# Kernel optimization log

Measured on AMD Instinct MI355X. Metric: run time of the kernel, lower is better.

## Reference

```python
import jax, jax.numpy as jnp
import numpy as np

VERY_NEG = -1e30
N_HEADS = 8


def _dag_attention(leaves, ancestors, mask, w1, b1, w2, b2):
    # leaves/ancestors: [C, A, H], mask: [C, A]
    m = mask[..., None]                                   # [C, A, 1]
    x = jnp.concatenate([leaves * m, ancestors * m], -1)  # [C, A, 2H]
    x = jax.nn.relu(x @ w1 + b1)                          # [C, A, H]
    s = x @ w2 + b2 + (1.0 - m) * VERY_NEG                # [C, A, 1]
    a = jax.nn.softmax(s, axis=1)
    return (a * ancestors * m).sum(axis=1)                # [C, H]


def _encoder_layer(x, mask4d, wq, wk, wv, wo, fw1, fb1, fw2, fb2):
    B, S, H = x.shape
    d = H // N_HEADS
    q = (x @ wq).reshape(B, S, N_HEADS, d)
    k = (x @ wk).reshape(B, S, N_HEADS, d)
    v = (x @ wv).reshape(B, S, N_HEADS, d)
    scores = jnp.einsum('bqhd,bkhd->bhqk', q, k) / jnp.sqrt(jnp.float32(d)) + mask4d
    attn = jax.nn.softmax(scores, axis=-1)
    ctx = jnp.einsum('bhqk,bkhd->bqhd', attn, v).reshape(B, S, H)
    x = x + ctx @ wo
    x = x + jax.nn.relu(x @ fw1 + fb1) @ fw2 + fb2
    return x


def _attention_pooling(x, mask3d, pw, pb):
    # x: [B, S, H], mask3d: [B, S, 1] additive mask
    s = x @ pw + pb + mask3d           # [B, S, 1]
    a = jax.nn.softmax(s, axis=1)
    return (a * x).sum(axis=1)          # [B, H]


def setup_inputs() -> dict:
    key = jax.random.key(0)
    ks = jax.random.split(key, 32)
    B, S, H, C, NODES, A = 128, 256, 256, 20000, 25000, 8

    def w(k, shape, scale=0.02):
        return (jax.random.normal(k, shape, jnp.float32) * scale)

    input_ids = jax.random.randint(ks[0], (B, S), 0, C)
    code_mask = (jax.random.uniform(ks[1], (B, S)) < 0.9).astype(jnp.float32)
    code_mask = code_mask.at[:, 0].set(1.0)
    dx_leaves_list = jax.random.randint(ks[2], (C, A), 0, NODES)
    dx_ancestors_list = jax.random.randint(ks[3], (C, A), 0, NODES)
    dx_masks_list = (jax.random.uniform(ks[4], (C, A)) < 0.8).astype(jnp.float32)
    dx_masks_list = dx_masks_list.at[:, 0].set(1.0)

    inp = dict(
        input_ids=input_ids, code_mask=code_mask,
        dx_leaves_list=dx_leaves_list, dx_ancestors_list=dx_ancestors_list,
        dx_masks_list=dx_masks_list,
        embed_init_w=w(ks[5], (NODES + 1, H)).at[NODES].set(0.0),  # padding row
        embed_inputs_w=w(ks[6], (C + 1, H)).at[C].set(0.0),
        attn_w1=w(ks[7], (2 * H, H)), attn_b1=jnp.zeros((H,), jnp.float32),
        attn_w2=w(ks[8], (H, 1)), attn_b2=jnp.zeros((1,), jnp.float32),
        pool_w=w(ks[9], (H, 1)), pool_b=jnp.zeros((1,), jnp.float32),
    )
    names = ['visit', 'dag']
    for i, nm in enumerate(names):
        base = 10 + 6 * i
        inp[nm + '_wq'] = w(ks[base], (H, H))
        inp[nm + '_wk'] = w(ks[base + 1], (H, H))
        inp[nm + '_wv'] = w(ks[base + 2], (H, H))
        inp[nm + '_wo'] = w(ks[base + 3], (H, H))
        inp[nm + '_fw1'] = w(ks[base + 4], (H, 4 * H))
        inp[nm + '_fb1'] = jnp.zeros((4 * H,), jnp.float32)
        inp[nm + '_fw2'] = w(ks[base + 5], (4 * H, H))
        inp[nm + '_fb2'] = jnp.zeros((H,), jnp.float32)
    return inp


def reference(input_ids, code_mask, dx_leaves_list, dx_ancestors_list, dx_masks_list,
              embed_init_w, embed_inputs_w, attn_w1, attn_b1, attn_w2, attn_b2,
              pool_w, pool_b,
              visit_wq, visit_wk, visit_wv, visit_wo, visit_fw1, visit_fb1, visit_fw2, visit_fb2,
              dag_wq, dag_wk, dag_wv, dag_wo, dag_fw1, dag_fb1, dag_fw2, dag_fb2):
    H = embed_init_w.shape[1]
    # Full-vocabulary DAG embedding recomputation (gather -> MLP -> masked softmax -> weighted sum)
    leaves_emb = embed_init_w[dx_leaves_list]          # [C, A, H]
    ancestors_emb = embed_init_w[dx_ancestors_list]    # [C, A, H]
    dag_emb = _dag_attention(leaves_emb, ancestors_emb, dx_masks_list,
                             attn_w1, attn_b1, attn_w2, attn_b2)   # [C, H]
    dict_matrix = jnp.concatenate([jnp.zeros((1, H), jnp.float32), dag_emb], axis=0)

    inputs = embed_inputs_w[input_ids]       # [B, S, H]
    inputs_dag = dict_matrix[input_ids]      # [B, S, H]

    ext_mask = (1.0 - code_mask)[:, None, None, :] * VERY_NEG  # [B,1,1,S]
    visit_outs = _encoder_layer(inputs, ext_mask, visit_wq, visit_wk, visit_wv, visit_wo,
                                visit_fw1, visit_fb1, visit_fw2, visit_fb2)
    dag_hidden = _encoder_layer(inputs_dag, ext_mask, dag_wq, dag_wk, dag_wv, dag_wo,
                                dag_fw1, dag_fb1, dag_fw2, dag_fb2)

    pool_mask = (1.0 - code_mask)[:, :, None] * VERY_NEG       # [B,S,1]
    dag_outs = _attention_pooling(dag_hidden, pool_mask, pool_w, pool_b)
    return (visit_outs, dag_outs)
```

## Files before the change

kernel.cpp:

```cpp
#include <hip/hip_runtime.h>
#include <hip/hip_bf16.h>
#include <math.h>

#define VERY_NEG (-1e30f)

constexpr int Bc = 128, Sc = 256, Hc = 256, Cc = 20000, Ac = 8, NHc = 8, DHc = 32, FFc = 1024;
constexpr int Mc = Bc * Sc;
constexpr int Rc = Cc * Ac;

typedef __attribute__((ext_vector_type(8))) short short8;
typedef __attribute__((ext_vector_type(4))) float floatx4;

static __device__ __forceinline__ unsigned short f2bf(float f) {
  union { float f; unsigned u; } v; v.f = f;
  unsigned r = v.u + 0x7FFF + ((v.u >> 16) & 1);
  return (unsigned short)(r >> 16);
}
static __device__ __forceinline__ unsigned pack2(float lo, float hi) {
  return (unsigned)f2bf(lo) | ((unsigned)f2bf(hi) << 16);
}
static __device__ __forceinline__ float bf2f(unsigned short u) {
  union { unsigned u; float f; } v; v.u = ((unsigned)u) << 16; return v.f;
}

static __device__ __forceinline__ void glds16(const unsigned short* g,
                                              unsigned short* l) {
  __builtin_amdgcn_global_load_lds(
      (const __attribute__((address_space(1))) void*)g,
      (__attribute__((address_space(3))) void*)l, 16, 0, 0);
}

__global__ __launch_bounds__(256) void prep_weights(
    const float* __restrict__ wq, const float* __restrict__ wk,
    const float* __restrict__ wv, const float* __restrict__ wo,
    const float* __restrict__ fw1, const float* __restrict__ fw2,
    unsigned short* __restrict__ qkvT, unsigned short* __restrict__ woT,
    unsigned short* __restrict__ fw1T, unsigned short* __restrict__ fw2T) {
  int gid = blockIdx.x * 256 + threadIdx.x;
  if (gid < 196608) {
    int which = gid >> 16, rem = gid & 65535;
    int n = rem >> 8, k = rem & 255;
    const float* w = which == 0 ? wq : (which == 1 ? wk : wv);
    qkvT[gid] = f2bf(w[k * 256 + n]);
  } else if (gid < 262144) {
    int rem = gid - 196608;
    int n = rem >> 8, k = rem & 255;
    woT[rem] = f2bf(wo[k * 256 + n]);
  } else if (gid < 524288) {
    int rem = gid - 262144;
    int n = rem >> 8, k = rem & 255;
    fw1T[rem] = f2bf(fw1[k * 1024 + n]);
  } else {
    int rem = gid - 524288;
    int n = rem >> 10, k = rem & 1023;
    fw2T[rem] = f2bf(fw2[k * 256 + n]);
  }
}

template <int K, bool BIAS, bool RELU, bool RESID, int OUT>
__global__ __launch_bounds__(256) void gemm_mfma(
    const unsigned short* __restrict__ A, const unsigned short* __restrict__ Bt,
    const float* __restrict__ bias, const float* __restrict__ resid,
    float* __restrict__ Cf, unsigned short* __restrict__ C2, int N) {
  __shared__ unsigned short As[128 * 64];
  __shared__ unsigned short Bs[128 * 64];
  const int tid = threadIdx.x;
  const int nwg = gridDim.x * gridDim.y;
  const int bid0 = blockIdx.y * gridDim.x + blockIdx.x;
  const int swz = (bid0 & 7) * (nwg >> 3) + (bid0 >> 3);
  const int rowBase = (swz / gridDim.x) * 128;
  const int colBase = (swz % gridDim.x) * 128;
  const int wave = tid >> 6, lane = tid & 63;
  const int wm = wave >> 1, wn = wave & 1;
  const int quad = lane >> 4, l15 = lane & 15;
  const int s8 = (((lane & 7) ^ (lane >> 3)) << 3);
  const int rs0 = (wave << 5) + (lane >> 3);
  const int swzf = l15 & 7;

  floatx4 acc[4][4];
#pragma unroll
  for (int mt = 0; mt < 4; ++mt)
#pragma unroll
    for (int nt = 0; nt < 4; ++nt) acc[mt][nt] = (floatx4){0.f, 0.f, 0.f, 0.f};

  for (int k0 = 0; k0 < K; k0 += 64) {
#pragma unroll
    for (int i = 0; i < 4; ++i) {
      int r = rs0 + (i << 3);
      int lb = wave * 2048 + i * 512;
      glds16(A + (size_t)(rowBase + r) * K + k0 + s8, &As[lb]);
      glds16(Bt + (size_t)(colBase + r) * K + k0 + s8, &Bs[lb]);
    }
    __syncthreads();
#pragma unroll
    for (int kk = 0; kk < 2; ++kk) {
      short8 af[4], bfr[4];
#pragma unroll
      for (int mt = 0; mt < 4; ++mt)
        af[mt] = *(const short8*)&As[(wm * 64 + mt * 16 + l15) * 64 +
                                     ((((kk << 2) | quad) ^ swzf) << 3)];
#pragma unroll
      for (int nt = 0; nt < 4; ++nt)
        bfr[nt] = *(const short8*)&Bs[(wn * 64 + nt * 16 + l15) * 64 +
                                      ((((kk << 2) | quad) ^ swzf) << 3)];
#pragma unroll
      for (int mt = 0; mt < 4; ++mt)
#pragma unroll
        for (int nt = 0; nt < 4; ++nt)
          acc[mt][nt] = __builtin_amdgcn_mfma_f32_16x16x32_bf16(
              af[mt], bfr[nt], acc[mt][nt], 0, 0, 0);
    }
    __syncthreads();
  }

#pragma unroll
  for (int mt = 0; mt < 4; ++mt) {
#pragma unroll
    for (int nt = 0; nt < 4; ++nt) {
      int col = colBase + wn * 64 + nt * 16 + l15;
      float bz = BIAS ? bias[col] : 0.f;
#pragma unroll
      for (int i = 0; i < 4; ++i) {
        int row = rowBase + wm * 64 + mt * 16 + quad * 4 + i;
        float v = acc[mt][nt][i];
        if (BIAS) v += bz;
        if (RELU) v = fmaxf(v, 0.f);
        if (RESID) v += resid[(size_t)row * N + col];
        if (OUT == 0) {
          Cf[(size_t)row * N + col] = v;
        } else if (OUT == 1) {
          C2[(size_t)row * N + col] = f2bf(v);
        } else if (OUT == 2) {
          Cf[(size_t)row * N + col] = v;
          C2[(size_t)row * N + col] = f2bf(v);
        } else {
          C2[(size_t)(col >> 8) * 16777216 + (size_t)row * 256 + (col & 255)] =
              f2bf(v);
        }
      }
    }
  }
}

__global__ __launch_bounds__(256) void cvt_emb16(
    const float* __restrict__ emb, unsigned short* __restrict__ e16) {
  int gid = blockIdx.x * 256 + threadIdx.x;
  int base = gid * 8;
  int row = base >> 8;
  uint4 o;
  if (row < 25001) {
    float4 a = *(const float4*)(emb + base);
    float4 b = *(const float4*)(emb + base + 4);
    o.x = pack2(a.x, a.y); o.y = pack2(a.z, a.w);
    o.z = pack2(b.x, b.y); o.w = pack2(b.z, b.w);
  } else {
    o = (uint4){0u, 0u, 0u, 0u};
  }
  *(uint4*)(e16 + base) = o;
}

__global__ __launch_bounds__(256) void prep_w1T_pq(
    const float* __restrict__ w1, unsigned short* __restrict__ Bt) {
  int gid = blockIdx.x * 256 + threadIdx.x;
  int n = gid >> 8, k = gid & 255;
  float v = (n < 256) ? w1[k * 256 + n] : w1[(256 + k) * 256 + (n - 256)];
  Bt[gid] = f2bf(v);
}

__global__ __launch_bounds__(256) void dag_score(
    const int* __restrict__ leaves, const int* __restrict__ anc,
    const unsigned short* __restrict__ PQ, const float* __restrict__ b1,
    const float* __restrict__ w2, float* __restrict__ s) {
  const int tid = threadIdx.x;
  const int l16 = tid & 15;
  const int r = blockIdx.x * 16 + (tid >> 4);

  float b1c[16], w2c[16];
#pragma unroll
  for (int j = 0; j < 4; ++j) {
    *(float4*)&b1c[j * 4] = *(const float4*)(b1 + l16 * 16 + j * 4);
    *(float4*)&w2c[j * 4] = *(const float4*)(w2 + l16 * 16 + j * 4);
  }

  const int nl = leaves[r], na = anc[r];
  const unsigned short* pp = PQ + (size_t)nl * 512 + l16 * 16;
  const unsigned short* qp = PQ + (size_t)na * 512 + 256 + l16 * 16;

  float acc = 0.f;
#pragma unroll
  for (int half = 0; half < 2; ++half) {
    uint4 pv = *(const uint4*)(pp + half * 8);
    uint4 qv = *(const uint4*)(qp + half * 8);
    const unsigned short* pu = (const unsigned short*)&pv;
    const unsigned short* qu = (const unsigned short*)&qv;
#pragma unroll
    for (int j = 0; j < 8; ++j) {
      float h = bf2f(pu[j]) + bf2f(qu[j]) + b1c[half * 8 + j];
      acc += fmaxf(h, 0.f) * w2c[half * 8 + j];
    }
  }
  acc += __shfl_xor(acc, 1, 64);
  acc += __shfl_xor(acc, 2, 64);
  acc += __shfl_xor(acc, 4, 64);
  acc += __shfl_xor(acc, 8, 64);
  if (l16 == 0) s[r] = acc;
}

__global__ __launch_bounds__(256) void dag_finalize(
    const float* __restrict__ s, const float* __restrict__ masks,
    const int* __restrict__ anc, const float* __restrict__ b2,
    const unsigned short* __restrict__ emb16, float* __restrict__ dict) {
  const int c = blockIdx.x;
  const int t = threadIdx.x;
  __shared__ float sv[8], mv[8];
  __shared__ int nv[8];
  if (t < 8) {
    int idx = c * 8 + t;
    float m = masks[idx];
    sv[t] = s[idx] + b2[0] + (1.f - m) * VERY_NEG;
    mv[t] = m;
    nv[t] = anc[idx];
  }
  __syncthreads();
  float mx = -INFINITY;
#pragma unroll
  for (int a = 0; a < 8; ++a) mx = fmaxf(mx, sv[a]);
  float e[8], sum = 0.f;
#pragma unroll
  for (int a = 0; a < 8; ++a) { e[a] = __expf(sv[a] - mx); sum += e[a]; }
  float inv = 1.f / sum;
  float o = 0.f;
#pragma unroll
  for (int a = 0; a < 8; ++a)
    o += e[a] * inv * mv[a] * bf2f(emb16[(size_t)nv[a] * 256 + t]);
  dict[(size_t)(c + 1) * 256 + t] = o;
  if (c == 0) dict[t] = 0.f;
}

__global__ __launch_bounds__(256) void gather_both(
    const int* __restrict__ ids, const float4* __restrict__ table,
    float4* __restrict__ outf, unsigned short* __restrict__ outb) {
  int gid = blockIdx.x * 256 + threadIdx.x;
  int row = gid >> 6;
  int c4 = gid & 63;
  float4 v = table[(size_t)ids[row] * 64 + c4];
  outf[gid] = v;
  uint2 o;
  o.x = pack2(v.x, v.y);
  o.y = pack2(v.z, v.w);
  *(uint2*)(outb + (size_t)gid * 4) = o;
}

static __device__ __forceinline__ int vt_addr(int d, int col) {
  return d * 272 + ((((col) * 2) ^ (((d >> 3) & 3) << 4)) >> 1);
}
static __device__ __forceinline__ int ps_addr(int row, int col) {
  return row * 40 + ((((col) * 2) ^ (((row >> 2) & 3) << 4)) >> 1);
}

__global__ __launch_bounds__(256, 4) void attn_mfma(
    const unsigned short* __restrict__ q, const unsigned short* __restrict__ k,
    const unsigned short* __restrict__ v, const float* __restrict__ cm,
    unsigned short* __restrict__ ctx) {
  __shared__ unsigned short Vt[32 * 272];
  __shared__ unsigned short Ps[4][64 * 40];
  __shared__ float madd[256];
  const int b = blockIdx.x >> 3, h = blockIdx.x & 7;
  const int tid = threadIdx.x;
  const int wave = tid >> 6, lane = tid & 63;
  const int quad = lane >> 4, l15 = lane & 15;
  const size_t tokbase = (size_t)b * 256;
  const int hoff = h * 32;

#pragma unroll
  for (int it = 0; it < 4; ++it) {
    int idx = tid + it * 256;
    int row = idx >> 2, c = idx & 3;
    uint4 w = *(const uint4*)(v + (tokbase + row) * 256 + hoff + c * 8);
    const unsigned short* wsp = (const unsigned short*)&w;
#pragma unroll
    for (int j = 0; j < 8; ++j) Vt[vt_addr(c * 8 + j, row)] = wsp[j];
  }
  madd[tid] = (1.f - cm[b * 256 + tid]) * VERY_NEG;
  __syncthreads();

  short8 qf[4];
#pragma unroll
  for (int mt = 0; mt < 4; ++mt) {
    size_t qrow = tokbase + wave * 64 + mt * 16 + l15;
    qf[mt] = *(const short8*)(q + qrow * 256 + hoff + quad * 8);
  }
  float madd_r[16];
#pragma unroll
  for (int nt = 0; nt < 16; ++nt) madd_r[nt] = madd[nt * 16 + l15];

  short8 vone;
#pragma unroll
  for (int j = 0; j < 8; ++j)
    ((unsigned short*)&vone)[j] = (l15 == 0) ? 0x3F80 : 0;

  floatx4 oa[4][2], oa_l[4];
#pragma unroll
  for (int mt = 0; mt < 4; ++mt) {
    oa_l[mt] = (floatx4){0.f, 0.f, 0.f, 0.f};
#pragma unroll
    for (int nd = 0; nd < 2; ++nd) oa[mt][nd] = (floatx4){0.f, 0.f, 0.f, 0.f};
  }

  const float scale = 0.17677669529663687f;
  unsigned short* Pw = &Ps[wave][0];

  for (int t = 0; t < 4; ++t) {
    short8 kf[4];
#pragma unroll
    for (int nt = 0; nt < 4; ++nt)
      kf[nt] = *(const short8*)(k + (tokbase + t * 64 + nt * 16 + l15) * 256 +
                                hoff + quad * 8);
    floatx4 sa[4][4];
#pragma unroll
    for (int mt = 0; mt < 4; ++mt)
#pragma unroll
      for (int nt = 0; nt < 4; ++nt) sa[mt][nt] = (floatx4){0.f, 0.f, 0.f, 0.f};
#pragma unroll
    for (int mt = 0; mt < 4; ++mt)
#pragma unroll
      for (int nt = 0; nt < 4; ++nt)
        sa[mt][nt] = __builtin_amdgcn_mfma_f32_16x16x32_bf16(
            qf[mt], kf[nt], sa[mt][nt], 0, 0, 0);

#pragma unroll
    for (int ks = 0; ks < 2; ++ks) {
#pragma unroll
      for (int mt = 0; mt < 4; ++mt)
#pragma unroll
        for (int n2 = 0; n2 < 2; ++n2) {
          int nt = ks * 2 + n2;
#pragma unroll
          for (int i = 0; i < 4; ++i) {
            float p = __expf(sa[mt][nt][i] * scale + madd_r[t * 4 + nt]);
            Pw[ps_addr(mt * 16 + quad * 4 + i, n2 * 16 + l15)] = f2bf(p);
          }
        }
      __asm__ __volatile__("s_waitcnt lgkmcnt(0)" ::: "memory");
      short8 vf[2];
#pragma unroll
      for (int nd = 0; nd < 2; ++nd)
        vf[nd] = *(const short8*)&Vt[vt_addr(nd * 16 + l15,
                                             t * 64 + ks * 32 + quad * 8)];
#pragma unroll
      for (int mt = 0; mt < 4; ++mt) {
        short8 pf = *(const short8*)&Pw[ps_addr(mt * 16 + l15, quad * 8)];
#pragma unroll
        for (int nd = 0; nd < 2; ++nd)
          oa[mt][nd] = __builtin_amdgcn_mfma_f32_16x16x32_bf16(
              pf, vf[nd], oa[mt][nd], 0, 0, 0);
        oa_l[mt] = __builtin_amdgcn_mfma_f32_16x16x32_bf16(
            pf, vone, oa_l[mt], 0, 0, 0);
      }
    }
  }

  float inv[4][4];
#pragma unroll
  for (int mt = 0; mt < 4; ++mt)
#pragma unroll
    for (int i = 0; i < 4; ++i) {
      float l = __shfl(oa_l[mt][i], lane & 48, 64);
      inv[mt][i] = 1.f / l;
    }
#pragma unroll
  for (int mt = 0; mt < 4; ++mt)
#pragma unroll
    for (int nd = 0; nd < 2; ++nd)
#pragma unroll
      for (int i = 0; i < 4; ++i)
        Pw[ps_addr(mt * 16 + quad * 4 + i, nd * 16 + l15)] =
            f2bf(oa[mt][nd][i] * inv[mt][i]);
  __asm__ __volatile__("s_waitcnt lgkmcnt(0)" ::: "memory");
#pragma unroll
  for (int it = 0; it < 4; ++it) {
    int idx = it * 64 + lane;
    int row = idx >> 2, c = idx & 3;
    uint4 w = *(const uint4*)&Pw[ps_addr(row, c * 8)];
    *(uint4*)(ctx + (tokbase + wave * 64 + row) * 256 + hoff + c * 8) = w;
  }
}

__global__ __launch_bounds__(256) void pool_kernel(
    const float* __restrict__ x, const float* __restrict__ code_mask,
    const float* __restrict__ pw, const float* __restrict__ pb,
    float* __restrict__ out) {
  const int b = blockIdx.x;
  const int t = threadIdx.x;
  __shared__ float ss[256];
  __shared__ float red[256];
  __shared__ float als[256];
  const float* xb = x + (size_t)b * 256 * 256;

  float s = pb[0];
  for (int j = 0; j < 256; j += 4) {
    float4 xv = *(const float4*)(xb + (size_t)t * 256 + j);
    float4 wv = *(const float4*)(pw + j);
    s += xv.x * wv.x + xv.y * wv.y + xv.z * wv.z + xv.w * wv.w;
  }
  s += (1.f - code_mask[b * 256 + t]) * VERY_NEG;
  ss[t] = s; red[t] = s;
  __syncthreads();
  for (int off = 128; off > 0; off >>= 1) {
    if (t < off) red[t] = fmaxf(red[t], red[t + off]);
    __syncthreads();
  }
  float m = red[0];
  __syncthreads();
  float e = __expf(ss[t] - m);
  als[t] = e; red[t] = e;
  __syncthreads();
  for (int off = 128; off > 0; off >>= 1) {
    if (t < off) red[t] += red[t + off];
    __syncthreads();
  }
  float inv = 1.f / red[0];
  float o = 0.f;
  for (int si = 0; si < 256; ++si) o += als[si] * xb[(size_t)si * 256 + t];
  out[b * 256 + t] = o * inv;
}

extern "C" void kernel_launch(void* const* d_in, const int* in_sizes, int n_in,
                              void* d_out, int out_size, void* d_ws,
                              size_t ws_size, hipStream_t stream) {
  const int* input_ids = (const int*)d_in[0];
  const float* code_mask = (const float*)d_in[1];
  const int* dx_leaves = (const int*)d_in[2];
  const int* dx_anc = (const int*)d_in[3];
  const float* dx_masks = (const float*)d_in[4];
  const float* embed_init_w = (const float*)d_in[5];
  const float* embed_inputs_w = (const float*)d_in[6];
  const float* attn_w1 = (const float*)d_in[7];
  const float* attn_b1 = (const float*)d_in[8];
  const float* attn_w2 = (const float*)d_in[9];
  const float* attn_b2 = (const float*)d_in[10];
  const float* pool_w = (const float*)d_in[11];
  const float* pool_b = (const float*)d_in[12];

  float* out = (float*)d_out;
  float* ws = (float*)d_ws;

  float* dict = ws;
  float* xbuf = dict + 5120256;
  float* qb   = xbuf + 8388608;
  float* kb   = qb + 8388608;
  float* vb   = kb + 8388608;
  float* ctxb = vb + 8388608;
  float* wend = ctxb + 8388608;

  unsigned short* emb16  = (unsigned short*)xbuf;
  unsigned short* pq16   = (unsigned short*)(xbuf + 3211264);
  unsigned short* w1T_pq = (unsigned short*)kb;
  float* sbuf = vb;

  unsigned short* xb16  = (unsigned short*)ctxb;
  unsigned short* qkv16 = (unsigned short*)qb;
  unsigned short* xq16  = (unsigned short*)qb;
  unsigned short* hid16 = (unsigned short*)kb;
  unsigned short* qkvT = (unsigned short*)wend;
  unsigned short* woT  = qkvT + 196608;
  unsigned short* fw1T = woT + 65536;
  unsigned short* fw2T = fw1T + 262144;

  cvt_emb16<<<3136, 256, 0, stream>>>(embed_init_w, emb16);
  prep_w1T_pq<<<512, 256, 0, stream>>>(attn_w1, w1T_pq);
  gemm_mfma<256, false, false, false, 1><<<dim3(4, 196), 256, 0, stream>>>(
      emb16, w1T_pq, nullptr, nullptr, nullptr, pq16, 512);
  dag_score<<<Rc / 16, 256, 0, stream>>>(dx_leaves, dx_anc, pq16, attn_b1,
                                         attn_w2, sbuf);
  dag_finalize<<<Cc, 256, 0, stream>>>(sbuf, dx_masks, dx_anc, attn_b2,
                                       emb16, dict);

  auto run_encoder = [&](const float* wq, const float* wk, const float* wv,
                         const float* wo, const float* fw1, const float* fb1,
                         const float* fw2, const float* fb2, float* final_out) {
    prep_weights<<<3072, 256, 0, stream>>>(wq, wk, wv, wo, fw1, fw2, qkvT,
                                           woT, fw1T, fw2T);
    gemm_mfma<256, false, false, false, 3><<<dim3(6, 256), 256, 0, stream>>>(
        xb16, qkvT, nullptr, nullptr, nullptr, qkv16, 256);
    attn_mfma<<<Bc * NHc, 256, 0, stream>>>(qkv16, qkv16 + 16777216,
                                            qkv16 + 33554432, code_mask, xb16);
    gemm_mfma<256, false, false, true, 2><<<dim3(2, 256), 256, 0, stream>>>(
        xb16, woT, nullptr, xbuf, xbuf, xq16, 256);
    gemm_mfma<256, true, true, false, 1><<<dim3(8, 256), 256, 0, stream>>>(
        xq16, fw1T, fb1, nullptr, nullptr, hid16, 1024);
    gemm_mfma<1024, true, false, true, 0><<<dim3(2, 256), 256, 0, stream>>>(
        hid16, fw2T, fb2, xbuf, final_out, nullptr, 256);
  };

  gather_both<<<8192, 256, 0, stream>>>(input_ids,
                                        (const float4*)embed_inputs_w,
                                        (float4*)xbuf, xb16);
  run_encoder((const float*)d_in[13], (const float*)d_in[14],
              (const float*)d_in[15], (const float*)d_in[16],
              (const float*)d_in[17], (const float*)d_in[18],
              (const float*)d_in[19], (const float*)d_in[20], out);

  gather_both<<<8192, 256, 0, stream>>>(input_ids, (const float4*)dict,
                                        (float4*)xbuf, xb16);
  run_encoder((const float*)d_in[21], (const float*)d_in[22],
              (const float*)d_in[23], (const float*)d_in[24],
              (const float*)d_in[25], (const float*)d_in[26],
              (const float*)d_in[27], (const float*)d_in[28], xbuf);

  pool_kernel<<<Bc, 256, 0, stream>>>(xbuf, code_mask, pool_w, pool_b,
                                      out + 8388608);
}
```

Baseline: 536.5 us.

## Fuse FFN up and down GEMMs into one kernel keeping hidden in LDS

Replaces the two FFN GEMM launches with a single kernel that computes each 128-row block's 1024-wide hidden activation in 128-column chunks, stores the chunk in shared memory, and immediately accumulates the down-projection. This removes the global write and re-read of the 32768x1024 bf16 hidden tensor. The cost is only 256 blocks at one block per CU with heavy register use (128 accumulator floats plus the hidden tile) and many barriers, so latency hiding is limited. The pooling kernel is also widened to 512 threads, splitting the weighted sum over sequence positions into two halves.

```diff
diff --git a/kernel.cpp b/kernel.cpp
--- a/kernel.cpp
+++ b/kernel.cpp
@@ -142,6 +142,158 @@
   }
 }
 
+__global__ __launch_bounds__(256, 1) void ffn_fused(
+    const unsigned short* __restrict__ A, const unsigned short* __restrict__ w1T,
+    const unsigned short* __restrict__ w2T, const float* __restrict__ b1,
+    const float* __restrict__ b2, const float* __restrict__ resid,
+    float* __restrict__ outC) {
+  __shared__ unsigned short Xs[4][8192];
+  __shared__ unsigned short Ws[2][8192];
+  __shared__ unsigned short Hs[2][8192];
+  const int tid = threadIdx.x;
+  const int wave = tid >> 6, lane = tid & 63;
+  const int wm = wave >> 1, wn = wave & 1;
+  const int quad = lane >> 4, l15 = lane & 15;
+  const int s8 = (((lane & 7) ^ (lane >> 3)) << 3);
+  const int rs0 = (wave << 5) + (lane >> 3);
+  const int rs0b = (wave << 6) + (lane >> 3);
+  const int swzf = l15 & 15 & 7;
+  const int rowBase = blockIdx.x * 128;
+
+#pragma unroll
+  for (int kc = 0; kc < 4; ++kc)
+#pragma unroll
+    for (int i = 0; i < 4; ++i) {
+      int r = rs0 + (i << 3);
+      glds16(A + (size_t)(rowBase + r) * 256 + kc * 64 + s8,
+             &Xs[kc][wave * 2048 + i * 512]);
+    }
+
+  floatx4 acc2[4][8];
+#pragma unroll
+  for (int mt = 0; mt < 4; ++mt)
+#pragma unroll
+    for (int nt = 0; nt < 8; ++nt) acc2[mt][nt] = (floatx4){0.f, 0.f, 0.f, 0.f};
+
+  for (int nb = 0; nb < 8; ++nb) {
+    floatx4 hacc[4][4];
+#pragma unroll
+    for (int mt = 0; mt < 4; ++mt)
+#pragma unroll
+      for (int nt = 0; nt < 4; ++nt) hacc[mt][nt] = (floatx4){0.f, 0.f, 0.f, 0.f};
+
+#pragma unroll
+    for (int hf = 0; hf < 2; ++hf) {
+#pragma unroll
+      for (int kc = 0; kc < 2; ++kc)
+#pragma unroll
+        for (int i = 0; i < 4; ++i) {
+          int r = rs0 + (i << 3);
+          glds16(w1T + (size_t)(nb * 128 + r) * 256 + (hf * 2 + kc) * 64 + s8,
+                 &Ws[kc][wave * 2048 + i * 512]);
+        }
+      __syncthreads();
+#pragma unroll
+      for (int kc = 0; kc < 2; ++kc) {
+        int kg = hf * 2 + kc;
+#pragma unroll
+        for (int kk = 0; kk < 2; ++kk) {
+          short8 af[4], bfr[4];
+#pragma unroll
+          for (int mt = 0; mt < 4; ++mt)
+            af[mt] = *(const short8*)&Xs[kg][(wm * 64 + mt * 16 + l15) * 64 +
+                                            ((((kk << 2) | quad) ^ swzf) << 3)];
+#pragma unroll
+          for (int nt = 0; nt < 4; ++nt)
+            bfr[nt] = *(const short8*)&Ws[kc][(wn * 64 + nt * 16 + l15) * 64 +
+                                             ((((kk << 2) | quad) ^ swzf) << 3)];
+#pragma unroll
+          for (int mt = 0; mt < 4; ++mt)
+#pragma unroll
+            for (int nt = 0; nt < 4; ++nt)
+              hacc[mt][nt] = __builtin_amdgcn_mfma_f32_16x16x32_bf16(
+                  af[mt], bfr[nt], hacc[mt][nt], 0, 0, 0);
+        }
+      }
+      __syncthreads();
+    }
+
+    float b1v[4];
+#pragma unroll
+    for (int nt = 0; nt < 4; ++nt)
+      b1v[nt] = b1[nb * 128 + wn * 64 + nt * 16 + l15];
+#pragma unroll
+    for (int mt = 0; mt < 4; ++mt)
+#pragma unroll
+      for (int nt = 0; nt < 4; ++nt) {
+        int nh = wn * 64 + nt * 16 + l15;
+        int kc2 = nh >> 6, c6 = nh & 63;
+#pragma unroll
+        for (int i = 0; i < 4; ++i) {
+          int row = wm * 64 + mt * 16 + quad * 4 + i;
+          float hv = fmaxf(hacc[mt][nt][i] + b1v[nt], 0.f);
+          Hs[kc2][row * 64 + ((((c6 >> 3) ^ (row & 7)) << 3) | (c6 & 7))] =
+              f2bf(hv);
+        }
+      }
+#pragma unroll
+    for (int i = 0; i < 8; ++i) {
+      int r = rs0b + (i << 3);
+      glds16(w2T + (size_t)r * 1024 + nb * 128 + s8,
+             &Ws[0][wave * 4096 + i * 512]);
+    }
+    __syncthreads();
+
+#pragma unroll
+    for (int kc2 = 0; kc2 < 2; ++kc2) {
+      if (kc2 == 1) {
+        __syncthreads();
+#pragma unroll
+        for (int i = 0; i < 8; ++i) {
+          int r = rs0b + (i << 3);
+          glds16(w2T + (size_t)r * 1024 + nb * 128 + 64 + s8,
+                 &Ws[0][wave * 4096 + i * 512]);
+        }
+        __syncthreads();
+      }
+#pragma unroll
+      for (int kk = 0; kk < 2; ++kk) {
+        short8 pf[4], bfr2[8];
+#pragma unroll
+        for (int mt = 0; mt < 4; ++mt)
+          pf[mt] = *(const short8*)&Hs[kc2][(wm * 64 + mt * 16 + l15) * 64 +
+                                           ((((kk << 2) | quad) ^ swzf) << 3)];
+        const unsigned short* W2f = &Ws[0][0];
+#pragma unroll
+        for (int nt = 0; nt < 8; ++nt)
+          bfr2[nt] = *(const short8*)&W2f[(wn * 128 + nt * 16 + l15) * 64 +
+                                          ((((kk << 2) | quad) ^ swzf) << 3)];
+#pragma unroll
+        for (int mt = 0; mt < 4; ++mt)
+#pragma unroll
+          for (int nt = 0; nt < 8; ++nt)
+            acc2[mt][nt] = __builtin_amdgcn_mfma_f32_16x16x32_bf16(
+                pf[mt], bfr2[nt], acc2[mt][nt], 0, 0, 0);
+      }
+    }
+    __syncthreads();
+  }
+
+#pragma unroll
+  for (int mt = 0; mt < 4; ++mt)
+#pragma unroll
+    for (int nt = 0; nt < 8; ++nt) {
+      int col = wn * 128 + nt * 16 + l15;
+      float bz = b2[col];
+#pragma unroll
+      for (int i = 0; i < 4; ++i) {
+        int row = rowBase + wm * 64 + mt * 16 + quad * 4 + i;
+        outC[(size_t)row * 256 + col] =
+            acc2[mt][nt][i] + bz + resid[(size_t)row * 256 + col];
+      }
+    }
+}
+
 __global__ __launch_bounds__(256) void cvt_emb16(
     const float* __restrict__ emb, unsigned short* __restrict__ e16) {
   int gid = blockIdx.x * 256 + threadIdx.x;
@@ -386,25 +538,29 @@
   }
 }
 
-__global__ __launch_bounds__(256) void pool_kernel(
+__global__ __launch_bounds__(512) void pool_kernel(
     const float* __restrict__ x, const float* __restrict__ code_mask,
     const float* __restrict__ pw, const float* __restrict__ pb,
     float* __restrict__ out) {
   const int b = blockIdx.x;
   const int t = threadIdx.x;
+  const int col = t & 255, half = t >> 8;
   __shared__ float ss[256];
   __shared__ float red[256];
   __shared__ float als[256];
+  __shared__ float osum[512];
   const float* xb = x + (size_t)b * 256 * 256;
 
-  float s = pb[0];
-  for (int j = 0; j < 256; j += 4) {
-    float4 xv = *(const float4*)(xb + (size_t)t * 256 + j);
-    float4 wv = *(const float4*)(pw + j);
-    s += xv.x * wv.x + xv.y * wv.y + xv.z * wv.z + xv.w * wv.w;
-  }
-  s += (1.f - code_mask[b * 256 + t]) * VERY_NEG;
-  ss[t] = s; red[t] = s;
+  if (t < 256) {
+    float s = pb[0];
+    for (int j = 0; j < 256; j += 4) {
+      float4 xv = *(const float4*)(xb + (size_t)t * 256 + j);
+      float4 wv = *(const float4*)(pw + j);
+      s += xv.x * wv.x + xv.y * wv.y + xv.z * wv.z + xv.w * wv.w;
+    }
+    s += (1.f - code_mask[b * 256 + t]) * VERY_NEG;
+    ss[t] = s; red[t] = s;
+  }
   __syncthreads();
   for (int off = 128; off > 0; off >>= 1) {
     if (t < off) red[t] = fmaxf(red[t], red[t + off]);
@@ -412,8 +568,10 @@
   }
   float m = red[0];
   __syncthreads();
-  float e = __expf(ss[t] - m);
-  als[t] = e; red[t] = e;
+  if (t < 256) {
+    float e = __expf(ss[t] - m);
+    als[t] = e; red[t] = e;
+  }
   __syncthreads();
   for (int off = 128; off > 0; off >>= 1) {
     if (t < off) red[t] += red[t + off];
@@ -421,8 +579,11 @@
   }
   float inv = 1.f / red[0];
   float o = 0.f;
-  for (int si = 0; si < 256; ++si) o += als[si] * xb[(size_t)si * 256 + t];
-  out[b * 256 + t] = o * inv;
+  for (int si = half * 128; si < half * 128 + 128; ++si)
+    o += als[si] * xb[(size_t)si * 256 + col];
+  osum[t] = o;
+  __syncthreads();
+  if (t < 256) out[b * 256 + t] = (osum[t] + osum[t + 256]) * inv;
 }
 
 extern "C" void kernel_launch(void* const* d_in, const int* in_sizes, int n_in,
@@ -461,7 +622,6 @@
   unsigned short* xb16  = (unsigned short*)ctxb;
   unsigned short* qkv16 = (unsigned short*)qb;
   unsigned short* xq16  = (unsigned short*)qb;
-  unsigned short* hid16 = (unsigned short*)kb;
   unsigned short* qkvT = (unsigned short*)wend;
   unsigned short* woT  = qkvT + 196608;
   unsigned short* fw1T = woT + 65536;
@@ -487,10 +647,8 @@
                                             qkv16 + 33554432, code_mask, xb16);
     gemm_mfma<256, false, false, true, 2><<<dim3(2, 256), 256, 0, stream>>>(
         xb16, woT, nullptr, xbuf, xbuf, xq16, 256);
-    gemm_mfma<256, true, true, false, 1><<<dim3(8, 256), 256, 0, stream>>>(
-        xq16, fw1T, fb1, nullptr, nullptr, hid16, 1024);
-    gemm_mfma<1024, true, false, true, 0><<<dim3(2, 256), 256, 0, stream>>>(
-        hid16, fw2T, fb2, xbuf, final_out, nullptr, 256);
+    ffn_fused<<<256, 256, 0, stream>>>(xq16, fw1T, fw2T, fb1, fb2, xbuf,
+                                       final_out);
   };
 
   gather_both<<<8192, 256, 0, stream>>>(input_ids,
@@ -508,6 +666,6 @@
               (const float*)d_in[25], (const float*)d_in[26],
               (const float*)d_in[27], (const float*)d_in[28], xbuf);
 
-  pool_kernel<<<Bc, 256, 0, stream>>>(xbuf, code_mask, pool_w, pool_b,
+  pool_kernel<<<Bc, 512, 0, stream>>>(xbuf, code_mask, pool_w, pool_b,
                                       out + 8388608);
 }
```

Result: slower. 567.3 us (+5.8%).
